# Optimization experiments

Hardware: AMD Instinct MI355X
Metric: run time of the kernel (lower is better)

The kernel has to match this reference:

```python
import jax, jax.numpy as jnp
import numpy as np

S = 4          # num_subspaces
H = 1024       # hidden_dim
D = H // S     # subspace_dim = 256
B, N = 8, 1024
EPS = 1e-8


def setup_inputs() -> dict:
    key = jax.random.key(0)
    ks = jax.random.split(key, 6)
    sp = 1.0 / np.sqrt(H).astype(np.float32)
    sr = 1.0 / np.sqrt(D).astype(np.float32)
    return {
        "hx": jax.random.normal(ks[0], (B, N, H), jnp.float32),
        "ha": jax.random.normal(ks[1], (B, N, H), jnp.float32),
        "Wp": jax.random.normal(ks[2], (S, H, D), jnp.float32) * sp,  # stacked subspace_projs
        "bp": jax.random.normal(ks[3], (S, D), jnp.float32) * 0.01,
        "Wr": jax.random.normal(ks[4], (S, D, H), jnp.float32) * sr,  # stacked subspace_reconstructs
        "br": jax.random.normal(ks[5], (S, H), jnp.float32) * 0.01,
    }


def reference(hx, ha, Wp, bp, Wr, br):
    # Project into all subspaces at once: [S, B, N, D]
    x_sub = jnp.einsum('bnh,shd->sbnd', hx, Wp) + bp[:, None, None, :]
    a_sub = jnp.einsum('bnh,shd->sbnd', ha, Wp) + bp[:, None, None, :]

    # Cosine similarity = dot product of L2-normalized vectors (eps-clamped norms)
    xn = x_sub / jnp.maximum(jnp.linalg.norm(x_sub, axis=-1, keepdims=True), EPS)
    an = a_sub / jnp.maximum(jnp.linalg.norm(a_sub, axis=-1, keepdims=True), EPS)
    sim = jnp.einsum('sbid,sbjd->sbij', xn, an)       # [S, B, Nx, Na]

    # Softmax across the subspace axis (torch stacks sims then softmax(dim=0))
    w = jax.nn.softmax(sim, axis=0)                   # [S, B, Nx, Na]

    # Weighted aggregation per subspace, then reconstruct and sum over subspaces
    weighted = jnp.einsum('sbij,sbjd->sbid', w, a_sub)          # [S, B, Nx, D]
    out = jnp.einsum('sbid,sdh->bih', weighted, Wr) + br.sum(axis=0)  # [B, Nx, H]
    return out
```

## Files before the change

### kernel.cpp

```cpp
#include <hip/hip_runtime.h>
#include <hip/hip_bf16.h>

#define S_ 4
#define H_ 1024
#define D_ 256
#define B_ 8
#define N_ 1024
#define R_ (B_*N_)
#define EPS_ 1e-8f

typedef float f32x4 __attribute__((ext_vector_type(4)));
typedef short bf16x8 __attribute__((ext_vector_type(8)));
typedef unsigned short u16;

__device__ __forceinline__ u16 f2b(float f) {
    union { __bf16 h; u16 u; } cv; cv.h = (__bf16)f; return cv.u;
}

__device__ __forceinline__ void gload16(const void* g, void* l) {
    __builtin_amdgcn_global_load_lds((const __attribute__((address_space(1))) void*)g,
                                     (__attribute__((address_space(3))) void*)l, 16, 0, 0);
}

__global__ __launch_bounds__(256) void k_cast8_2(const float* __restrict__ hx,
                                                 const float* __restrict__ ha,
                                                 u16* __restrict__ hxb, u16* __restrict__ hab,
                                                 int n8) {
    int i = blockIdx.x * 256 + threadIdx.x;
    const float* src; u16* dst;
    if (i < n8) { src = hx; dst = hxb; } else { src = ha; dst = hab; i -= n8; }
    const float4 v0 = ((const float4*)src)[2 * i];
    const float4 v1 = ((const float4*)src)[2 * i + 1];
    union { u16 u[8]; uint4 v; } o;
    o.u[0] = f2b(v0.x); o.u[1] = f2b(v0.y); o.u[2] = f2b(v0.z); o.u[3] = f2b(v0.w);
    o.u[4] = f2b(v1.x); o.u[5] = f2b(v1.y); o.u[6] = f2b(v1.z); o.u[7] = f2b(v1.w);
    ((uint4*)dst)[i] = o.v;
}

__device__ __forceinline__ void tc64(const float* __restrict__ src, int lds_,
                                     u16* __restrict__ dst, int ldd) {
    __shared__ float t[64][65];
    const int tid = threadIdx.x;
    const int rr = tid >> 4;
    const int cc = (tid & 15) * 4;
    #pragma unroll
    for (int p = 0; p < 4; ++p) {
        const int r = rr + p * 16;
        const float4 v = *(const float4*)(src + (size_t)r * lds_ + cc);
        t[r][cc] = v.x; t[r][cc + 1] = v.y; t[r][cc + 2] = v.z; t[r][cc + 3] = v.w;
    }
    __syncthreads();
    #pragma unroll
    for (int p = 0; p < 4; ++p) {
        const int c = rr + p * 16;
        union { u16 u[4]; uint2 v; } o;
        o.u[0] = f2b(t[cc + 0][c]); o.u[1] = f2b(t[cc + 1][c]);
        o.u[2] = f2b(t[cc + 2][c]); o.u[3] = f2b(t[cc + 3][c]);
        *(uint2*)(dst + (size_t)c * ldd + cc) = o.v;
    }
}

__global__ __launch_bounds__(256) void k_tc_wp(const float* __restrict__ Wp, u16* __restrict__ WpT) {
    const int s = blockIdx.z;
    const int r0 = blockIdx.x * 64;
    const int c0 = blockIdx.y * 64;
    tc64(Wp + (size_t)s * H_ * D_ + (size_t)r0 * D_ + c0, D_,
         WpT + (size_t)s * D_ * H_ + (size_t)c0 * H_ + r0, H_);
}

__global__ __launch_bounds__(256) void k_tc_wr(const float* __restrict__ Wr, u16* __restrict__ WrT) {
    const int r0 = blockIdx.y * 64;
    const int c0 = blockIdx.x * 64;
    tc64(Wr + (size_t)r0 * H_ + c0, H_,
         WrT + (size_t)c0 * H_ + r0, H_);
}

__global__ __launch_bounds__(256) void k_brsum(const float* __restrict__ br, float* __restrict__ bs) {
    const int h = blockIdx.x * 256 + threadIdx.x;
    if (h < H_) bs[h] = br[h] + br[H_ + h] + br[2 * H_ + h] + br[3 * H_ + h];
}

__global__ __launch_bounds__(256) void k_tc_araw(const u16* __restrict__ src, u16* __restrict__ dst) {
    const int sb = blockIdx.z, s = sb >> 3, b = sb & 7;
    const int j0 = blockIdx.x * 64, d0 = blockIdx.y * 64;
    __shared__ u16 tile[64][68];
    const int t = threadIdx.x;
    const int r = t >> 4, c4 = (t & 15) * 4;
    #pragma unroll
    for (int p = 0; p < 4; ++p) {
        const int row = p * 16 + r;
        *(uint2*)&tile[row][c4] =
            *(const uint2*)(src + (size_t)(b * N_ + j0 + row) * 1024 + s * 256 + d0 + c4);
    }
    __syncthreads();
    #pragma unroll
    for (int p = 0; p < 4; ++p) {
        const int orow = p * 16 + r;
        union { u16 u[4]; uint2 v; } o;
        o.u[0] = tile[c4 + 0][orow]; o.u[1] = tile[c4 + 1][orow];
        o.u[2] = tile[c4 + 2][orow]; o.u[3] = tile[c4 + 3][orow];
        *(uint2*)(dst + ((size_t)sb << 18) + (size_t)(d0 + orow) * 1024 + j0 + c4) = o.v;
    }
}

template<int WROWS, int WCOLS, int MFR, int NFR>
__device__ __forceinline__ void gemm_dbuf(
    const u16* __restrict__ Ag, const u16* __restrict__ Bg,
    int lda, int ldb, int K, u16* SA, u16* SB, f32x4 (&acc)[MFR][NFR])
{
    constexpr int NT = WROWS * WCOLS * 64;
    constexpr int TM = WROWS * MFR * 16;
    constexpr int TN = WCOLS * NFR * 16;
    constexpr int CA = TM * 8 / NT;
    constexpr int CB = TN * 8 / NT;
    constexpr int L  = CA + CB;
    const int tid = threadIdx.x, l = tid & 63, wv = tid >> 6;
    const int wm = wv / WCOLS, wn = wv % WCOLS;
    const int nsteps = K / 64;

    auto STAGE = [&](int buf, int k0) {
        #pragma unroll
        for (int i = 0; i < CA; ++i) {
            const int ci = i * NT + tid;
            const int row = ci >> 3, c = ci & 7, cs = c ^ (row & 7);
            gload16(Ag + (size_t)row * lda + k0 + cs * 8, SA + buf * TM * 64 + ci * 8);
        }
        #pragma unroll
        for (int i = 0; i < CB; ++i) {
            const int ci = i * NT + tid;
            const int row = ci >> 3, c = ci & 7, cs = c ^ (row & 7);
            gload16(Bg + (size_t)row * ldb + k0 + cs * 8, SB + buf * TN * 64 + ci * 8);
        }
    };

    STAGE(0, 0);
    for (int t = 0; t < nsteps; ++t) {
        const int cur = t & 1;
        if (t < nsteps - 1) {
            STAGE(cur ^ 1, (t + 1) * 64);
            if constexpr (L == 3)      asm volatile("s_waitcnt vmcnt(3)" ::: "memory");
            else if constexpr (L == 6) asm volatile("s_waitcnt vmcnt(6)" ::: "memory");
            else if constexpr (L == 8) asm volatile("s_waitcnt vmcnt(8)" ::: "memory");
            else                       asm volatile("s_waitcnt vmcnt(0)" ::: "memory");
        } else {
            asm volatile("s_waitcnt vmcnt(0)" ::: "memory");
        }
        __builtin_amdgcn_s_barrier();
        __builtin_amdgcn_sched_barrier(0);
        bf16x8 af[2][MFR], bq[2][NFR];
        #pragma unroll
        for (int kc = 0; kc < 2; ++kc) {
            #pragma unroll
            for (int m = 0; m < MFR; ++m) {
                const int r = wm * MFR * 16 + m * 16 + (l & 15);
                const int c = (kc * 4 + (l >> 4)) ^ (r & 7);
                af[kc][m] = *(const bf16x8*)(SA + cur * TM * 64 + r * 64 + c * 8);
            }
            #pragma unroll
            for (int n = 0; n < NFR; ++n) {
                const int r = wn * NFR * 16 + n * 16 + (l & 15);
                const int c = (kc * 4 + (l >> 4)) ^ (r & 7);
                bq[kc][n] = *(const bf16x8*)(SB + cur * TN * 64 + r * 64 + c * 8);
            }
        }
        asm volatile("s_waitcnt lgkmcnt(0)" ::: "memory");
        __builtin_amdgcn_s_barrier();
        __builtin_amdgcn_sched_barrier(0);
        #pragma unroll
        for (int kc = 0; kc < 2; ++kc)
            #pragma unroll
            for (int m = 0; m < MFR; ++m)
                #pragma unroll
                for (int n = 0; n < NFR; ++n)
                    acc[m][n] = __builtin_amdgcn_mfma_f32_16x16x32_bf16(af[kc][m], bq[kc][n], acc[m][n], 0, 0, 0);
    }
}

__global__ __launch_bounds__(512, 4) void k_proj_norm(
    const u16* __restrict__ hxb, const u16* __restrict__ hab,
    const u16* __restrict__ WpT, const float* __restrict__ bp,
    u16* __restrict__ xnb, u16* __restrict__ araw, float* __restrict__ inv_na)
{
    __shared__ u16 SA[2 * 128 * 32];
    __shared__ u16 SB[2 * 256 * 32];
    __shared__ float normbuf[128][4];

    const int is_a = blockIdx.z;
    const int s  = blockIdx.y;
    const int rt = blockIdx.x * 128;
    const int tid = threadIdx.x;
    const int l = tid & 63, wv = tid >> 6;
    const int wm = wv >> 2, wn = wv & 3;
    const u16* __restrict__ Ag = (is_a ? hab : hxb) + (size_t)rt * 1024;
    const u16* __restrict__ Bg = WpT + (size_t)(s * 256) * 1024;

    f32x4 acc[4][4];
    #pragma unroll
    for (int m = 0; m < 4; ++m)
        #pragma unroll
        for (int n = 0; n < 4; ++n) acc[m][n] = (f32x4){0.f, 0.f, 0.f, 0.f};

    auto STAGE = [&](int buf, int k0) {
        {
            const int ci = tid;
            const int row = ci >> 2, c = ci & 3, cs = (c - (row >> 1)) & 3;
            gload16(Ag + (size_t)row * 1024 + k0 + cs * 8, SA + buf * 4096 + ci * 8);
        }
        #pragma unroll
        for (int i = 0; i < 2; ++i) {
            const int ci = i * 512 + tid;
            const int row = ci >> 2, c = ci & 3, cs = (c - (row >> 1)) & 3;
            gload16(Bg + (size_t)row * 1024 + k0 + cs * 8, SB + buf * 8192 + ci * 8);
        }
    };

    STAGE(0, 0);
    for (int t = 0; t < 32; ++t) {
        const int cur = t & 1;
        if (t < 31) {
            STAGE(cur ^ 1, (t + 1) * 32);
            asm volatile("s_waitcnt vmcnt(3)" ::: "memory");
        } else {
            asm volatile("s_waitcnt vmcnt(0)" ::: "memory");
        }
        __builtin_amdgcn_s_barrier();
        __builtin_amdgcn_sched_barrier(0);
        bf16x8 af[4], bq[4];
        #pragma unroll
        for (int m = 0; m < 4; ++m) {
            const int r = wm * 64 + m * 16 + (l & 15);
            const int c = ((l >> 4) + (r >> 1)) & 3;
            af[m] = *(const bf16x8*)(SA + cur * 4096 + r * 32 + c * 8);
        }
        #pragma unroll
        for (int n = 0; n < 4; ++n) {
            const int r = wn * 64 + n * 16 + (l & 15);
            const int c = ((l >> 4) + (r >> 1)) & 3;
            bq[n] = *(const bf16x8*)(SB + cur * 8192 + r * 32 + c * 8);
        }
        asm volatile("s_waitcnt lgkmcnt(0)" ::: "memory");
        __builtin_amdgcn_s_barrier();
        __builtin_amdgcn_sched_barrier(0);
        #pragma unroll
        for (int m = 0; m < 4; ++m)
            #pragma unroll
            for (int n = 0; n < 4; ++n)
                acc[m][n] = __builtin_amdgcn_mfma_f32_16x16x32_bf16(af[m], bq[n], acc[m][n], 0, 0, 0);
    }

    float bv[4];
    #pragma unroll
    for (int n = 0; n < 4; ++n) bv[n] = bp[s * 256 + wn * 64 + n * 16 + (l & 15)];
    #pragma unroll
    for (int m = 0; m < 4; ++m)
        #pragma unroll
        for (int n = 0; n < 4; ++n)
            #pragma unroll
            for (int q = 0; q < 4; ++q) acc[m][n][q] += bv[n];

    float ss[4][4];
    #pragma unroll
    for (int m = 0; m < 4; ++m)
        #pragma unroll
        for (int q = 0; q < 4; ++q) {
            float v = 0.f;
            #pragma unroll
            for (int n = 0; n < 4; ++n) v += acc[m][n][q] * acc[m][n][q];
            ss[m][q] = v;
        }
    #pragma unroll
    for (int off = 1; off <= 8; off <<= 1)
        #pragma unroll
        for (int m = 0; m < 4; ++m)
            #pragma unroll
            for (int q = 0; q < 4; ++q) ss[m][q] += __shfl_xor(ss[m][q], off, 64);
    if ((l & 15) == 0) {
        #pragma unroll
        for (int m = 0; m < 4; ++m)
            #pragma unroll
            for (int q = 0; q < 4; ++q)
                normbuf[wm * 64 + m * 16 + (l >> 4) * 4 + q][wn] = ss[m][q];
    }
    __syncthreads();
    float sc[4][4];
    #pragma unroll
    for (int m = 0; m < 4; ++m)
        #pragma unroll
        for (int q = 0; q < 4; ++q) {
            const int rl = wm * 64 + m * 16 + (l >> 4) * 4 + q;
            const float tot = normbuf[rl][0] + normbuf[rl][1] + normbuf[rl][2] + normbuf[rl][3];
            sc[m][q] = 1.0f / fmaxf(sqrtf(tot), EPS_);
        }
    if (!is_a) {
        #pragma unroll
        for (int m = 0; m < 4; ++m)
            #pragma unroll
            for (int n = 0; n < 4; ++n)
                #pragma unroll
                for (int q = 0; q < 4; ++q) {
                    const int rl = wm * 64 + m * 16 + (l >> 4) * 4 + q;
                    xnb[(size_t)(rt + rl) * 1024 + s * 256 + wn * 64 + n * 16 + (l & 15)] =
                        f2b(acc[m][n][q] * sc[m][q]);
                }
    } else {
        #pragma unroll
        for (int m = 0; m < 4; ++m)
            #pragma unroll
            for (int n = 0; n < 4; ++n)
                #pragma unroll
                for (int q = 0; q < 4; ++q) {
                    const int rl = wm * 64 + m * 16 + (l >> 4) * 4 + q;
                    araw[(size_t)(rt + rl) * 1024 + s * 256 + wn * 64 + n * 16 + (l & 15)] =
                        f2b(acc[m][n][q]);
                }
        if (wn == 0 && (l & 15) == 0) {
            #pragma unroll
            for (int m = 0; m < 4; ++m)
                #pragma unroll
                for (int q = 0; q < 4; ++q) {
                    const int rl = wm * 64 + m * 16 + (l >> 4) * 4 + q;
                    inv_na[s * R_ + rt + rl] = sc[m][q];
                }
        }
    }
}

__global__ __launch_bounds__(512, 4) void k_sim_v3(
    const u16* __restrict__ xnb, const u16* __restrict__ araw,
    const float* __restrict__ inv_na, u16* __restrict__ whalf, const int half)
{
    __shared__ u16 SmA[2 * 64 * 64];
    __shared__ u16 SmB[2 * 128 * 64];
    const int b   = blockIdx.z;
    const int itl = blockIdx.y * 64;
    const int it  = half * 512 + itl;
    const int jt  = blockIdx.x * 128;
    const int tid = threadIdx.x, l = tid & 63, wv = tid >> 6;
    const int wi = wv >> 2, wj = wv & 3;
    const u16* __restrict__ Ag = xnb  + (size_t)(b * N_ + it) * 1024;
    const u16* __restrict__ Bg = araw + (size_t)(b * N_ + jt) * 1024;

    f32x4 acc[4][2][2];
    #pragma unroll
    for (int s = 0; s < 4; ++s)
        #pragma unroll
        for (int m = 0; m < 2; ++m)
            #pragma unroll
            for (int n = 0; n < 2; ++n) acc[s][m][n] = (f32x4){0.f, 0.f, 0.f, 0.f};

    auto STAGE = [&](int buf, int t) {
        const int k0 = t * 64;
        {
            const int ci = tid;
            const int row = ci >> 3, c = ci & 7, cs = c ^ (row & 7);
            gload16(Ag + (size_t)row * 1024 + k0 + cs * 8, SmA + buf * 4096 + ci * 8);
        }
        #pragma unroll
        for (int i = 0; i < 2; ++i) {
            const int ci = i * 512 + tid;
            const int row = ci >> 3, c = ci & 7, cs = c ^ (row & 7);
            gload16(Bg + (size_t)row * 1024 + k0 + cs * 8, SmB + buf * 8192 + ci * 8);
        }
    };

    STAGE(0, 0);
    #pragma unroll
    for (int s = 0; s < 4; ++s) {
        #pragma unroll
        for (int kk = 0; kk < 4; ++kk) {
            const int t = s * 4 + kk;
            const int cur = t & 1;
            if (t < 15) {
                STAGE(cur ^ 1, t + 1);
                asm volatile("s_waitcnt vmcnt(3)" ::: "memory");
            } else {
                asm volatile("s_waitcnt vmcnt(0)" ::: "memory");
            }
            __builtin_amdgcn_s_barrier();
            __builtin_amdgcn_sched_barrier(0);
            bf16x8 af[2][2], bq[2][2];
            #pragma unroll
            for (int kc = 0; kc < 2; ++kc) {
                #pragma unroll
                for (int m = 0; m < 2; ++m) {
                    const int r = wi * 32 + m * 16 + (l & 15);
                    const int c = (kc * 4 + (l >> 4)) ^ (r & 7);
                    af[kc][m] = *(const bf16x8*)(SmA + cur * 4096 + r * 64 + c * 8);
                }
                #pragma unroll
                for (int n = 0; n < 2; ++n) {
                    const int r = wj * 32 + n * 16 + (l & 15);
                    const int c = (kc * 4 + (l >> 4)) ^ (r & 7);
                    bq[kc][n] = *(const bf16x8*)(SmB + cur * 8192 + r * 64 + c * 8);
                }
            }
            asm volatile("s_waitcnt lgkmcnt(0)" ::: "memory");
            __builtin_amdgcn_s_barrier();
            __builtin_amdgcn_sched_barrier(0);
            #pragma unroll
            for (int kc = 0; kc < 2; ++kc)
                #pragma unroll
                for (int m = 0; m < 2; ++m)
                    #pragma unroll
                    for (int n = 0; n < 2; ++n)
                        acc[s][m][n] = __builtin_amdgcn_mfma_f32_16x16x32_bf16(
                            af[kc][m], bq[kc][n], acc[s][m][n], 0, 0, 0);
        }
    }

    #pragma unroll
    for (int n = 0; n < 2; ++n) {
        const int jg = jt + wj * 32 + n * 16 + (l & 15);
        float inv[4];
        #pragma unroll
        for (int s = 0; s < 4; ++s) inv[s] = inv_na[s * R_ + b * N_ + jg];
        #pragma unroll
        for (int m = 0; m < 2; ++m)
            #pragma unroll
            for (int q = 0; q < 4; ++q) {
                const int il = itl + wi * 32 + m * 16 + (l >> 4) * 4 + q;
                float e[4]; float sum = 0.f;
                #pragma unroll
                for (int s = 0; s < 4; ++s) { e[s] = __expf(acc[s][m][n][q] * inv[s]); sum += e[s]; }
                const float rs = 1.0f / sum;
                #pragma unroll
                for (int s = 0; s < 4; ++s)
                    whalf[((size_t)(s * B_ + b) << 19) + (size_t)il * 1024 + jg] = f2b(e[s] * rs);
            }
    }
}

__global__ __launch_bounds__(256, 2) void k_gemm_weighted(
    const u16* __restrict__ whalf, const u16* __restrict__ arawT,
    u16* __restrict__ weighted, const int half)
{
    __shared__ u16 SA[2 * 64 * 64];
    __shared__ u16 SB[2 * 128 * 64];
    const int sb = blockIdx.z, s = sb >> 3, b = sb & 7;
    const int mt = blockIdx.y * 64, nt = blockIdx.x * 128;
    f32x4 acc[2][4];
    #pragma unroll
    for (int m = 0; m < 2; ++m)
        #pragma unroll
        for (int n = 0; n < 4; ++n) acc[m][n] = (f32x4){0.f, 0.f, 0.f, 0.f};
    gemm_dbuf<2, 2, 2, 4>(whalf + ((size_t)sb << 19) + (size_t)mt * 1024,
                          arawT + ((size_t)sb << 18) + (size_t)nt * 1024,
                          1024, 1024, 1024, SA, SB, acc);
    const int l = threadIdx.x & 63, wv = threadIdx.x >> 6;
    const int wm = wv >> 1, wn = wv & 1;
    #pragma unroll
    for (int m = 0; m < 2; ++m)
        #pragma unroll
        for (int n = 0; n < 4; ++n)
            #pragma unroll
            for (int q = 0; q < 4; ++q) {
                const int i = half * 512 + mt + wm * 32 + m * 16 + (l >> 4) * 4 + q;
                const int d = nt + wn * 64 + n * 16 + (l & 15);
                weighted[(size_t)(b * N_ + i) * 1024 + s * 256 + d] = f2b(acc[m][n][q]);
            }
}

__global__ __launch_bounds__(256, 2) void k_gemm_recon(
    const u16* __restrict__ weighted, const u16* __restrict__ WrT,
    const float* __restrict__ brsum, float* __restrict__ out)
{
    __shared__ u16 SA[2 * 128 * 64];
    __shared__ u16 SB[2 * 128 * 64];
    const int mt = blockIdx.y * 128, nt = blockIdx.x * 128;
    f32x4 acc[4][4];
    #pragma unroll
    for (int m = 0; m < 4; ++m)
        #pragma unroll
        for (int n = 0; n < 4; ++n) acc[m][n] = (f32x4){0.f, 0.f, 0.f, 0.f};
    gemm_dbuf<2, 2, 4, 4>(weighted + (size_t)mt * 1024, WrT + (size_t)nt * 1024,
                          1024, 1024, 1024, SA, SB, acc);
    const int l = threadIdx.x & 63, wv = threadIdx.x >> 6;
    const int wm = wv >> 1, wn = wv & 1;
    #pragma unroll
    for (int m = 0; m < 4; ++m)
        #pragma unroll
        for (int n = 0; n < 4; ++n)
            #pragma unroll
            for (int q = 0; q < 4; ++q) {
                const int row = mt + wm * 64 + m * 16 + (l >> 4) * 4 + q;
                const int col = nt + wn * 64 + n * 16 + (l & 15);
                out[(size_t)row * 1024 + col] = acc[m][n][q] + brsum[col];
            }
}

extern "C" void kernel_launch(void* const* d_in, const int* in_sizes, int n_in,
                              void* d_out, int out_size, void* d_ws, size_t ws_size,
                              hipStream_t stream) {
    const float* hx = (const float*)d_in[0];
    const float* ha = (const float*)d_in[1];
    const float* Wp = (const float*)d_in[2];
    const float* bp = (const float*)d_in[3];
    const float* Wr = (const float*)d_in[4];
    const float* br = (const float*)d_in[5];
    float* out = (float*)d_out;

    char* W = (char*)d_ws;
    u16* hxb      = (u16*)(W);
    u16* hab      = (u16*)(W + (16ull << 20));
    u16* WpT      = (u16*)(W + (32ull << 20));
    u16* WrT      = (u16*)(W + (34ull << 20));
    float* brsum  = (float*)(W + (36ull << 20));
    float* inv_na = (float*)(W + (36ull << 20) + (256ull << 10));
    u16* xnb      = (u16*)(W + (37ull << 20));
    u16* araw     = (u16*)(W + (53ull << 20));
    u16* arawT    = (u16*)(W + (69ull << 20));
    u16* whalf    = (u16*)(W + (85ull << 20));
    u16* weighted = (u16*)(W);

    k_cast8_2<<<dim3(2 * R_ * H_ / 8 / 256), dim3(256), 0, stream>>>(hx, ha, hxb, hab, R_ * H_ / 8);
    k_tc_wp<<<dim3(16, 4, 4), dim3(256), 0, stream>>>(Wp, WpT);
    k_tc_wr<<<dim3(16, 16), dim3(256), 0, stream>>>(Wr, WrT);
    k_brsum<<<dim3(4), dim3(256), 0, stream>>>(br, brsum);

    k_proj_norm<<<dim3(64, 4, 2), dim3(512), 0, stream>>>(hxb, hab, WpT, bp, xnb, araw, inv_na);

    k_tc_araw<<<dim3(16, 4, 32), dim3(256), 0, stream>>>(araw, arawT);

    for (int half = 0; half < 2; ++half) {
        k_sim_v3<<<dim3(8, 8, 8), dim3(512), 0, stream>>>(xnb, araw, inv_na, whalf, half);
        k_gemm_weighted<<<dim3(2, 8, 32), dim3(256), 0, stream>>>(whalf, arawT, weighted, half);
    }

    k_gemm_recon<<<dim3(8, 64), dim3(256), 0, stream>>>(weighted, WrT, brsum, out);
}
```

Measured before the change: 185.4 us.

## Fuse fp32-to-bf16 input cast into projection GEMM A-tile staging

Removes the separate cast kernel that converted hx/ha to bf16 in workspace; the projection GEMM now loads fp32 A tiles into registers, converts them to bf16 and writes them to LDS, while B still uses direct global-to-LDS loads. The A loads are software-pipelined two k-steps ahead using register double buffers and explicit vmcnt waits. This drops a 64MB read plus 32MB write pass and a launch. In exchange the GEMM reads fp32 inputs four times over (once per subspace block), which doubles A traffic per block, and the conversion adds VALU work inside the main loop.

Result: faster. 178.2 us (-3.9%).

```diff
diff --git a/kernel.cpp b/kernel.cpp
--- a/kernel.cpp
+++ b/kernel.cpp
@@ -20,21 +20,6 @@
 __device__ __forceinline__ void gload16(const void* g, void* l) {
     __builtin_amdgcn_global_load_lds((const __attribute__((address_space(1))) void*)g,
                                      (__attribute__((address_space(3))) void*)l, 16, 0, 0);
-}
-
-__global__ __launch_bounds__(256) void k_cast8_2(const float* __restrict__ hx,
-                                                 const float* __restrict__ ha,
-                                                 u16* __restrict__ hxb, u16* __restrict__ hab,
-                                                 int n8) {
-    int i = blockIdx.x * 256 + threadIdx.x;
-    const float* src; u16* dst;
-    if (i < n8) { src = hx; dst = hxb; } else { src = ha; dst = hab; i -= n8; }
-    const float4 v0 = ((const float4*)src)[2 * i];
-    const float4 v1 = ((const float4*)src)[2 * i + 1];
-    union { u16 u[8]; uint4 v; } o;
-    o.u[0] = f2b(v0.x); o.u[1] = f2b(v0.y); o.u[2] = f2b(v0.z); o.u[3] = f2b(v0.w);
-    o.u[4] = f2b(v1.x); o.u[5] = f2b(v1.y); o.u[6] = f2b(v1.z); o.u[7] = f2b(v1.w);
-    ((uint4*)dst)[i] = o.v;
 }
 
 __device__ __forceinline__ void tc64(const float* __restrict__ src, int lds_,
@@ -177,12 +162,12 @@
 }
 
 __global__ __launch_bounds__(512, 4) void k_proj_norm(
-    const u16* __restrict__ hxb, const u16* __restrict__ hab,
+    const float* __restrict__ hx, const float* __restrict__ ha,
     const u16* __restrict__ WpT, const float* __restrict__ bp,
     u16* __restrict__ xnb, u16* __restrict__ araw, float* __restrict__ inv_na)
 {
-    __shared__ u16 SA[2 * 128 * 32];
-    __shared__ u16 SB[2 * 256 * 32];
+    __shared__ u16 SA[2][128][32];
+    __shared__ u16 SB[2][256][32];
     __shared__ float normbuf[128][4];
 
     const int is_a = blockIdx.z;
@@ -191,54 +176,54 @@
     const int tid = threadIdx.x;
     const int l = tid & 63, wv = tid >> 6;
     const int wm = wv >> 2, wn = wv & 3;
-    const u16* __restrict__ Ag = (is_a ? hab : hxb) + (size_t)rt * 1024;
+    const float* __restrict__ Ag = (is_a ? ha : hx) + (size_t)rt * 1024;
     const u16* __restrict__ Bg = WpT + (size_t)(s * 256) * 1024;
 
+    const int arow = tid >> 2, aslot = tid & 3;
+    const int acs  = (aslot - (arow >> 1)) & 3;
+    const float* __restrict__ Ap = Ag + (size_t)arow * 1024 + acs * 8;
+
     f32x4 acc[4][4];
     #pragma unroll
     for (int m = 0; m < 4; ++m)
         #pragma unroll
         for (int n = 0; n < 4; ++n) acc[m][n] = (f32x4){0.f, 0.f, 0.f, 0.f};
 
-    auto STAGE = [&](int buf, int k0) {
-        {
-            const int ci = tid;
-            const int row = ci >> 2, c = ci & 3, cs = (c - (row >> 1)) & 3;
-            gload16(Ag + (size_t)row * 1024 + k0 + cs * 8, SA + buf * 4096 + ci * 8);
-        }
+    float4 a0[2], a1[2];
+    auto ALOAD = [&](float4 (&r)[2], int k0) {
+        r[0] = *(const float4*)(Ap + k0);
+        r[1] = *(const float4*)(Ap + k0 + 4);
+    };
+    auto AWRITE = [&](const float4 (&r)[2], int buf) {
+        union { u16 u[8]; uint4 v; } o;
+        o.u[0] = f2b(r[0].x); o.u[1] = f2b(r[0].y); o.u[2] = f2b(r[0].z); o.u[3] = f2b(r[0].w);
+        o.u[4] = f2b(r[1].x); o.u[5] = f2b(r[1].y); o.u[6] = f2b(r[1].z); o.u[7] = f2b(r[1].w);
+        *(uint4*)&SA[buf][arow][aslot * 8] = o.v;
+    };
+    auto BSTAGE = [&](int buf, int k0) {
         #pragma unroll
         for (int i = 0; i < 2; ++i) {
             const int ci = i * 512 + tid;
             const int row = ci >> 2, c = ci & 3, cs = (c - (row >> 1)) & 3;
-            gload16(Bg + (size_t)row * 1024 + k0 + cs * 8, SB + buf * 8192 + ci * 8);
-        }
-    };
-
-    STAGE(0, 0);
-    for (int t = 0; t < 32; ++t) {
-        const int cur = t & 1;
-        if (t < 31) {
-            STAGE(cur ^ 1, (t + 1) * 32);
-            asm volatile("s_waitcnt vmcnt(3)" ::: "memory");
-        } else {
-            asm volatile("s_waitcnt vmcnt(0)" ::: "memory");
-        }
-        __builtin_amdgcn_s_barrier();
-        __builtin_amdgcn_sched_barrier(0);
+            gload16(Bg + (size_t)row * 1024 + k0 + cs * 8, &SB[buf][row][c * 8]);
+        }
+    };
+    auto COMPUTE = [&](int cur) {
         bf16x8 af[4], bq[4];
         #pragma unroll
         for (int m = 0; m < 4; ++m) {
             const int r = wm * 64 + m * 16 + (l & 15);
             const int c = ((l >> 4) + (r >> 1)) & 3;
-            af[m] = *(const bf16x8*)(SA + cur * 4096 + r * 32 + c * 8);
+            af[m] = *(const bf16x8*)&SA[cur][r][c * 8];
         }
         #pragma unroll
         for (int n = 0; n < 4; ++n) {
             const int r = wn * 64 + n * 16 + (l & 15);
             const int c = ((l >> 4) + (r >> 1)) & 3;
-            bq[n] = *(const bf16x8*)(SB + cur * 8192 + r * 32 + c * 8);
+            bq[n] = *(const bf16x8*)&SB[cur][r][c * 8];
         }
         asm volatile("s_waitcnt lgkmcnt(0)" ::: "memory");
+        __builtin_amdgcn_sched_barrier(0);
         __builtin_amdgcn_s_barrier();
         __builtin_amdgcn_sched_barrier(0);
         #pragma unroll
@@ -246,7 +231,40 @@
             #pragma unroll
             for (int n = 0; n < 4; ++n)
                 acc[m][n] = __builtin_amdgcn_mfma_f32_16x16x32_bf16(af[m], bq[n], acc[m][n], 0, 0, 0);
-    }
+    };
+    auto BODY = [&](int t, float4 (&wset)[2], float4 (&lset)[2], int cur, bool doload) {
+        asm volatile("s_waitcnt vmcnt(2)" ::: "memory");
+        __builtin_amdgcn_sched_barrier(0);
+        AWRITE(wset, cur ^ 1);
+        if (doload) ALOAD(lset, (t + 2) * 32);
+        BSTAGE(cur ^ 1, (t + 1) * 32);
+        if (doload) asm volatile("s_waitcnt vmcnt(4)" ::: "memory");
+        else        asm volatile("s_waitcnt vmcnt(2)" ::: "memory");
+        asm volatile("s_waitcnt lgkmcnt(0)" ::: "memory");
+        __builtin_amdgcn_sched_barrier(0);
+        __builtin_amdgcn_s_barrier();
+        __builtin_amdgcn_sched_barrier(0);
+        COMPUTE(cur);
+    };
+
+    ALOAD(a0, 0);
+    ALOAD(a1, 32);
+    BSTAGE(0, 0);
+    asm volatile("s_waitcnt vmcnt(4)" ::: "memory");
+    __builtin_amdgcn_sched_barrier(0);
+    AWRITE(a0, 0);
+
+    for (int tt = 0; tt < 30; tt += 2) {
+        BODY(tt,     a1, a0, 0, true);
+        BODY(tt + 1, a0, a1, 1, true);
+    }
+    BODY(30, a1, a0, 0, false);
+    asm volatile("s_waitcnt vmcnt(0)" ::: "memory");
+    asm volatile("s_waitcnt lgkmcnt(0)" ::: "memory");
+    __builtin_amdgcn_sched_barrier(0);
+    __builtin_amdgcn_s_barrier();
+    __builtin_amdgcn_sched_barrier(0);
+    COMPUTE(1);
 
     float bv[4];
     #pragma unroll
@@ -500,8 +518,6 @@
     float* out = (float*)d_out;
 
     char* W = (char*)d_ws;
-    u16* hxb      = (u16*)(W);
-    u16* hab      = (u16*)(W + (16ull << 20));
     u16* WpT      = (u16*)(W + (32ull << 20));
     u16* WrT      = (u16*)(W + (34ull << 20));
     float* brsum  = (float*)(W + (36ull << 20));
@@ -512,12 +528,11 @@
     u16* whalf    = (u16*)(W + (85ull << 20));
     u16* weighted = (u16*)(W);
 
-    k_cast8_2<<<dim3(2 * R_ * H_ / 8 / 256), dim3(256), 0, stream>>>(hx, ha, hxb, hab, R_ * H_ / 8);
     k_tc_wp<<<dim3(16, 4, 4), dim3(256), 0, stream>>>(Wp, WpT);
     k_tc_wr<<<dim3(16, 16), dim3(256), 0, stream>>>(Wr, WrT);
     k_brsum<<<dim3(4), dim3(256), 0, stream>>>(br, brsum);
 
-    k_proj_norm<<<dim3(64, 4, 2), dim3(512), 0, stream>>>(hxb, hab, WpT, bp, xnb, araw, inv_na);
+    k_proj_norm<<<dim3(64, 4, 2), dim3(512), 0, stream>>>(hx, ha, WpT, bp, xnb, araw, inv_na);
 
     k_tc_araw<<<dim3(16, 4, 32), dim3(256), 0, stream>>>(araw, arawT);
 
```
